# Performance work log

Hardware: AMD Instinct MI355X
Metric: run time of the kernel (lower is better)

Reference implementation:

```python
import jax, jax.numpy as jnp
import numpy as np

B, H, I = 64, 4096, 14336   # batch, hidden, expert intermediate
NLUT = 4096                 # 2**L_bits, L=12
W_SCALE = 0.02              # payload['W_scale'] (same for all three here)


def _rademacher(key, shape):
    return jnp.where(jax.random.bernoulli(key, 0.5, shape), 1.0, -1.0).astype(jnp.float32)


def setup_inputs() -> dict:
    key = jax.random.key(0)
    ks = jax.random.split(key, 14)
    inp = {
        "x": jax.random.normal(ks[0], (B, H), jnp.float32),
        "lut_gate": jax.random.normal(ks[1], (NLUT,), jnp.float32) * 0.05,
        "lut_up": jax.random.normal(ks[2], (NLUT,), jnp.float32) * 0.05,
        "lut_down": jax.random.normal(ks[3], (NLUT,), jnp.float32) * 0.05,
        "gate_walks": jax.random.randint(ks[4], (I, H), 0, NLUT, jnp.int32),
        "up_walks": jax.random.randint(ks[5], (I, H), 0, NLUT, jnp.int32),
        "down_walks": jax.random.randint(ks[6], (H, I), 0, NLUT, jnp.int32),
        "gate_sign_l": _rademacher(ks[7], (I,)),
        "gate_sign_r": _rademacher(ks[8], (H,)),
        "up_sign_l": _rademacher(ks[9], (I,)),
        "up_sign_r": _rademacher(ks[10], (H,)),
        "down_sign_l": _rademacher(ks[11], (H,)),
        "down_sign_r": _rademacher(ks[12], (I,)),
    }
    return inp


def _dequant(lut, walks, sign_l, sign_r):
    # trellis-walk LUT gather per weight element, then row/col signs and scalar scale
    # walks: (out, in) int codes; lut: (NLUT,)
    return (lut[walks] * sign_l[:, None] * sign_r[None, :]) * W_SCALE


def reference(x, lut_gate, lut_up, lut_down,
              gate_walks, up_walks, down_walks,
              gate_sign_l, gate_sign_r, up_sign_l, up_sign_r,
              down_sign_l, down_sign_r):
    W_gate = _dequant(lut_gate, gate_walks, gate_sign_l, gate_sign_r)  # (I, H)
    W_up = _dequant(lut_up, up_walks, up_sign_l, up_sign_r)            # (I, H)
    W_down = _dequant(lut_down, down_walks, down_sign_l, down_sign_r)  # (H, I)
    gate_out = jax.nn.silu(x @ W_gate.T)   # (B, I)
    up_out = x @ W_up.T                    # (B, I)
    hidden = gate_out * up_out
    return hidden @ W_down.T               # (B, H)
```

## Files before the change

kernel.cpp:

```cpp
#include <hip/hip_runtime.h>
#include <hip/hip_bf16.h>

#define HD   4096
#define ID   14336
#define NB   64
#define NLUTN 4096
#define GU_KS 4
#define D_KS  16

typedef __attribute__((ext_vector_type(8))) short short8;
typedef __attribute__((ext_vector_type(4))) float f32x4;

__device__ __forceinline__ unsigned short f2bf(float f) {
  __hip_bfloat16 h = __float2bfloat16(f);
  return __builtin_bit_cast(unsigned short, h);
}

__device__ __forceinline__ void g2l16(const unsigned short* g, unsigned short* l) {
  __builtin_amdgcn_global_load_lds(
      (const __attribute__((address_space(1))) unsigned int*)g,
      (__attribute__((address_space(3))) unsigned int*)l, 16, 0, 0);
}

__global__ __launch_bounds__(256) void prep_kernel(
    const float* __restrict__ x, const float* __restrict__ gsr,
    const float* __restrict__ usr,
    unsigned short* __restrict__ xg, unsigned short* __restrict__ xu)
{
  int t = blockIdx.x * 256 + threadIdx.x;
  float4 xv = ((const float4*)x)[t];
  int hs = t & (HD/4 - 1);
  float4 g = ((const float4*)gsr)[hs];
  float4 u = ((const float4*)usr)[hs];
  ((ushort4*)xg)[t] = make_ushort4(f2bf(xv.x*g.x), f2bf(xv.y*g.y), f2bf(xv.z*g.z), f2bf(xv.w*g.w));
  ((ushort4*)xu)[t] = make_ushort4(f2bf(xv.x*u.x), f2bf(xv.y*u.y), f2bf(xv.z*u.z), f2bf(xv.w*u.w));
}

__global__ __launch_bounds__(256, 4) void gate_up_kernel(
    const int* __restrict__ gw, const int* __restrict__ uw,
    const float* __restrict__ lutg_f, const float* __restrict__ lutu_f,
    const unsigned short* __restrict__ xg, const unsigned short* __restrict__ xu,
    float* __restrict__ pg, float* __restrict__ pu)
{
  __shared__ unsigned short lutg[NLUTN];
  __shared__ unsigned short lutu[NLUTN];
  __shared__ unsigned short Bg[2][64*32];
  __shared__ unsigned short Bu[2][64*32];

  const int tid = threadIdx.x;
  #pragma unroll
  for (int i = tid; i < NLUTN/4; i += 256) {
    float4 g = ((const float4*)lutg_f)[i];
    float4 u = ((const float4*)lutu_f)[i];
    ((ushort4*)lutg)[i] = make_ushort4(f2bf(g.x), f2bf(g.y), f2bf(g.z), f2bf(g.w));
    ((ushort4*)lutu)[i] = make_ushort4(f2bf(u.x), f2bf(u.y), f2bf(u.z), f2bf(u.w));
  }

  const int lane = tid & 63;
  const int wv   = tid >> 6;
  const int col  = lane & 15;
  const int quad = lane >> 4;
  const int m0   = blockIdx.x * 64;
  const int mrow0 = m0 + wv * 16;
  const int kb   = blockIdx.y * (HD / GU_KS);
  const int KC   = HD / GU_KS;

  const int srow = 16*wv + (lane >> 2);
  const int soff = (lane & 3) * 8;
  const unsigned short* xgs = xg + (size_t)srow * HD + kb + soff;
  const unsigned short* xus = xu + (size_t)srow * HD + kb + soff;

  const int* gp = gw + (size_t)(mrow0 + col) * HD + kb + quad * 8;
  const int* up = uw + (size_t)(mrow0 + col) * HD + kb + quad * 8;

  g2l16(xgs, &Bg[0][wv*512]);
  g2l16(xus, &Bu[0][wv*512]);
  int4 ga = *(const int4*)(gp);
  int4 gb = *(const int4*)(gp + 4);
  int4 ua = *(const int4*)(up);
  int4 ub = *(const int4*)(up + 4);
  __syncthreads();

  const f32x4 z = {0.f, 0.f, 0.f, 0.f};
  f32x4 accg[4] = {z, z, z, z};
  f32x4 accu[4] = {z, z, z, z};

  for (int k0 = 0; k0 < KC; k0 += 32) {
    const int buf = (k0 >> 5) & 1;
    const int kn = k0 + 32;
    if (kn < KC) {
      g2l16(xgs + kn, &Bg[buf^1][wv*512]);
      g2l16(xus + kn, &Bu[buf^1][wv*512]);
    }
    int4 cga = ga, cgb = gb, cua = ua, cub = ub;
    const int knw = (kn < KC) ? kn : 0;
    ga = *(const int4*)(gp + knw);
    gb = *(const int4*)(gp + knw + 4);
    ua = *(const int4*)(up + knw);
    ub = *(const int4*)(up + knw + 4);

    short8 afg, afu;
    afg[0] = (short)lutg[cga.x]; afg[1] = (short)lutg[cga.y];
    afg[2] = (short)lutg[cga.z]; afg[3] = (short)lutg[cga.w];
    afg[4] = (short)lutg[cgb.x]; afg[5] = (short)lutg[cgb.y];
    afg[6] = (short)lutg[cgb.z]; afg[7] = (short)lutg[cgb.w];
    afu[0] = (short)lutu[cua.x]; afu[1] = (short)lutu[cua.y];
    afu[2] = (short)lutu[cua.z]; afu[3] = (short)lutu[cua.w];
    afu[4] = (short)lutu[cub.x]; afu[5] = (short)lutu[cub.y];
    afu[6] = (short)lutu[cub.z]; afu[7] = (short)lutu[cub.w];

    #pragma unroll
    for (int t = 0; t < 4; ++t) {
      short8 bgf = *(const short8*)&Bg[buf][(t*16 + col)*32 + quad*8];
      short8 buf_ = *(const short8*)&Bu[buf][(t*16 + col)*32 + quad*8];
      accg[t] = __builtin_amdgcn_mfma_f32_16x16x32_bf16(afg, bgf, accg[t], 0, 0, 0);
      accu[t] = __builtin_amdgcn_mfma_f32_16x16x32_bf16(afu, buf_, accu[t], 0, 0, 0);
    }
    __syncthreads();
  }

  const int irow = mrow0 + quad * 4;
  #pragma unroll
  for (int t = 0; t < 4; ++t) {
    const int b = t*16 + col;
    float* pgb = pg + (size_t)b * ID + irow;
    float* pub = pu + (size_t)b * ID + irow;
    #pragma unroll
    for (int r = 0; r < 4; ++r) {
      atomicAdd(pgb + r, accg[t][r]);
      atomicAdd(pub + r, accu[t][r]);
    }
  }
}

__global__ __launch_bounds__(256) void hidden_kernel(
    const float* __restrict__ pg, const float* __restrict__ pu,
    const float* __restrict__ gsl, const float* __restrict__ usl,
    const float* __restrict__ dsr,
    unsigned short* __restrict__ hidden)
{
  const int t = blockIdx.x * 256 + threadIdx.x;
  const int I4 = ID / 4;
  const int b = t / I4, i4 = t % I4;
  float4 g4 = ((const float4*)pg)[(size_t)b * I4 + i4];
  float4 u4 = ((const float4*)pu)[(size_t)b * I4 + i4];
  float4 sg = ((const float4*)gsl)[i4];
  float4 su = ((const float4*)usl)[i4];
  float4 sd = ((const float4*)dsr)[i4];
  float g0 = g4.x * 0.02f * sg.x, u0 = u4.x * 0.02f * su.x;
  float g1 = g4.y * 0.02f * sg.y, u1 = u4.y * 0.02f * su.y;
  float g2 = g4.z * 0.02f * sg.z, u2 = u4.z * 0.02f * su.z;
  float g3 = g4.w * 0.02f * sg.w, u3 = u4.w * 0.02f * su.w;
  ushort4 hv;
  hv.x = f2bf((g0 / (1.f + __expf(-g0))) * u0 * sd.x);
  hv.y = f2bf((g1 / (1.f + __expf(-g1))) * u1 * sd.y);
  hv.z = f2bf((g2 / (1.f + __expf(-g2))) * u2 * sd.z);
  hv.w = f2bf((g3 / (1.f + __expf(-g3))) * u3 * sd.w);
  ((ushort4*)hidden)[(size_t)b * I4 + i4] = hv;
}

__global__ __launch_bounds__(256, 4) void down_kernel(
    const int* __restrict__ dw, const float* __restrict__ lutd_f,
    const unsigned short* __restrict__ hidden,
    const float* __restrict__ dsl,
    float* __restrict__ out)
{
  __shared__ unsigned short lutd[NLUTN];
  __shared__ unsigned short Bh[2][64*32];

  const int tid = threadIdx.x;
  #pragma unroll
  for (int i = tid; i < NLUTN/4; i += 256) {
    float4 d = ((const float4*)lutd_f)[i];
    ((ushort4*)lutd)[i] = make_ushort4(f2bf(d.x), f2bf(d.y), f2bf(d.z), f2bf(d.w));
  }

  const int lane = tid & 63;
  const int wv   = tid >> 6;
  const int col  = lane & 15;
  const int quad = lane >> 4;
  const int m0   = blockIdx.x * 64;
  const int mrow0 = m0 + wv * 16;
  const int kb   = blockIdx.y * (ID / D_KS);
  const int KC   = ID / D_KS;

  const int srow = 16*wv + (lane >> 2);
  const int soff = (lane & 3) * 8;
  const unsigned short* hsrc = hidden + (size_t)srow * ID + kb + soff;

  const int* dp = dw + (size_t)(mrow0 + col) * ID + kb + quad * 8;

  g2l16(hsrc, &Bh[0][wv*512]);
  int4 da = *(const int4*)(dp);
  int4 db = *(const int4*)(dp + 4);
  __syncthreads();

  const f32x4 z = {0.f, 0.f, 0.f, 0.f};
  f32x4 acc[4] = {z, z, z, z};

  for (int k0 = 0; k0 < KC; k0 += 32) {
    const int buf = (k0 >> 5) & 1;
    const int kn = k0 + 32;
    if (kn < KC) g2l16(hsrc + kn, &Bh[buf^1][wv*512]);
    int4 cda = da, cdb = db;
    const int knw = (kn < KC) ? kn : 0;
    da = *(const int4*)(dp + knw);
    db = *(const int4*)(dp + knw + 4);

    short8 af;
    af[0] = (short)lutd[cda.x]; af[1] = (short)lutd[cda.y];
    af[2] = (short)lutd[cda.z]; af[3] = (short)lutd[cda.w];
    af[4] = (short)lutd[cdb.x]; af[5] = (short)lutd[cdb.y];
    af[6] = (short)lutd[cdb.z]; af[7] = (short)lutd[cdb.w];

    #pragma unroll
    for (int t = 0; t < 4; ++t) {
      short8 bh = *(const short8*)&Bh[buf][(t*16 + col)*32 + quad*8];
      acc[t] = __builtin_amdgcn_mfma_f32_16x16x32_bf16(af, bh, acc[t], 0, 0, 0);
    }
    __syncthreads();
  }

  const int hrow = mrow0 + quad * 4;
  float sc[4];
  #pragma unroll
  for (int r = 0; r < 4; ++r) sc[r] = 0.02f * dsl[hrow + r];
  #pragma unroll
  for (int t = 0; t < 4; ++t) {
    const int b = t*16 + col;
    float* ob = out + (size_t)b * HD + hrow;
    #pragma unroll
    for (int r = 0; r < 4; ++r)
      atomicAdd(ob + r, acc[t][r] * sc[r]);
  }
}

extern "C" void kernel_launch(void* const* d_in, const int* in_sizes, int n_in,
                              void* d_out, int out_size, void* d_ws, size_t ws_size,
                              hipStream_t stream) {
  const float* x    = (const float*)d_in[0];
  const float* lutg = (const float*)d_in[1];
  const float* lutu = (const float*)d_in[2];
  const float* lutd = (const float*)d_in[3];
  const int*   gw   = (const int*)d_in[4];
  const int*   uw   = (const int*)d_in[5];
  const int*   dw   = (const int*)d_in[6];
  const float* gsl  = (const float*)d_in[7];
  const float* gsr  = (const float*)d_in[8];
  const float* usl  = (const float*)d_in[9];
  const float* usr  = (const float*)d_in[10];
  const float* dsl  = (const float*)d_in[11];
  const float* dsr  = (const float*)d_in[12];
  float* out = (float*)d_out;

  unsigned short* xg     = (unsigned short*)d_ws;
  unsigned short* xu     = xg + (size_t)NB * HD;
  unsigned short* hidden = xu + (size_t)NB * HD;
  float* pg = (float*)(hidden + (size_t)NB * ID);
  float* pu = pg + (size_t)NB * ID;

  hipMemsetAsync(d_out, 0, (size_t)NB * HD * sizeof(float), stream);
  hipMemsetAsync(pg, 0, (size_t)2 * NB * ID * sizeof(float), stream);
  prep_kernel<<<(NB*HD/4 + 255)/256, 256, 0, stream>>>(x, gsr, usr, xg, xu);
  gate_up_kernel<<<dim3(ID/64, GU_KS), 256, 0, stream>>>(gw, uw, lutg, lutu,
                                                         xg, xu, pg, pu);
  hidden_kernel<<<(NB*ID/4 + 255)/256, 256, 0, stream>>>(pg, pu, gsl, usl, dsr,
                                                         hidden);
  down_kernel<<<dim3(HD/64, D_KS), 256, 0, stream>>>(dw, lutd, hidden, dsl, out);
}
```

Baseline: 757.6 us.

## Load activation fragments directly from global into registers, drop LDS staging and barriers

The gate/up and down kernels no longer stage activation tiles through double-buffered shared memory with global_load_lds. Each lane now reads its MFMA B-operand fragments straight from global memory into registers, prefetching the next k-step while the MFMAs run. This removes the per-iteration __syncthreads and the LDS traffic. In exchange every wave loads the full 64-row activation tile itself, so global/L2 reads go up by the number of waves per block, and register pressure rises. A barrier is added after the LUT fill so the lookups read a fully written table.

```diff
diff --git a/kernel.cpp b/kernel.cpp
--- a/kernel.cpp
+++ b/kernel.cpp
@@ -14,12 +14,6 @@
 __device__ __forceinline__ unsigned short f2bf(float f) {
   __hip_bfloat16 h = __float2bfloat16(f);
   return __builtin_bit_cast(unsigned short, h);
-}
-
-__device__ __forceinline__ void g2l16(const unsigned short* g, unsigned short* l) {
-  __builtin_amdgcn_global_load_lds(
-      (const __attribute__((address_space(1))) unsigned int*)g,
-      (__attribute__((address_space(3))) unsigned int*)l, 16, 0, 0);
 }
 
 __global__ __launch_bounds__(256) void prep_kernel(
@@ -44,8 +38,6 @@
 {
   __shared__ unsigned short lutg[NLUTN];
   __shared__ unsigned short lutu[NLUTN];
-  __shared__ unsigned short Bg[2][64*32];
-  __shared__ unsigned short Bu[2][64*32];
 
   const int tid = threadIdx.x;
   #pragma unroll
@@ -55,6 +47,7 @@
     ((ushort4*)lutg)[i] = make_ushort4(f2bf(g.x), f2bf(g.y), f2bf(g.z), f2bf(g.w));
     ((ushort4*)lutu)[i] = make_ushort4(f2bf(u.x), f2bf(u.y), f2bf(u.z), f2bf(u.w));
   }
+  __syncthreads();
 
   const int lane = tid & 63;
   const int wv   = tid >> 6;
@@ -65,58 +58,55 @@
   const int kb   = blockIdx.y * (HD / GU_KS);
   const int KC   = HD / GU_KS;
 
-  const int srow = 16*wv + (lane >> 2);
-  const int soff = (lane & 3) * 8;
-  const unsigned short* xgs = xg + (size_t)srow * HD + kb + soff;
-  const unsigned short* xus = xu + (size_t)srow * HD + kb + soff;
-
   const int* gp = gw + (size_t)(mrow0 + col) * HD + kb + quad * 8;
   const int* up = uw + (size_t)(mrow0 + col) * HD + kb + quad * 8;
-
-  g2l16(xgs, &Bg[0][wv*512]);
-  g2l16(xus, &Bu[0][wv*512]);
+  const unsigned short* xgp[4];
+  const unsigned short* xup[4];
+  #pragma unroll
+  for (int t = 0; t < 4; ++t) {
+    xgp[t] = xg + (size_t)(t*16 + col) * HD + kb + quad * 8;
+    xup[t] = xu + (size_t)(t*16 + col) * HD + kb + quad * 8;
+  }
+
   int4 ga = *(const int4*)(gp);
   int4 gb = *(const int4*)(gp + 4);
   int4 ua = *(const int4*)(up);
   int4 ub = *(const int4*)(up + 4);
-  __syncthreads();
+  short8 bgr[4], bur[4];
+  #pragma unroll
+  for (int t = 0; t < 4; ++t) {
+    bgr[t] = __builtin_bit_cast(short8, *(const int4*)(xgp[t]));
+    bur[t] = __builtin_bit_cast(short8, *(const int4*)(xup[t]));
+  }
 
   const f32x4 z = {0.f, 0.f, 0.f, 0.f};
   f32x4 accg[4] = {z, z, z, z};
   f32x4 accu[4] = {z, z, z, z};
 
   for (int k0 = 0; k0 < KC; k0 += 32) {
-    const int buf = (k0 >> 5) & 1;
-    const int kn = k0 + 32;
-    if (kn < KC) {
-      g2l16(xgs + kn, &Bg[buf^1][wv*512]);
-      g2l16(xus + kn, &Bu[buf^1][wv*512]);
+    short8 afg, afu;
+    afg[0] = (short)lutg[ga.x]; afg[1] = (short)lutg[ga.y];
+    afg[2] = (short)lutg[ga.z]; afg[3] = (short)lutg[ga.w];
+    afg[4] = (short)lutg[gb.x]; afg[5] = (short)lutg[gb.y];
+    afg[6] = (short)lutg[gb.z]; afg[7] = (short)lutg[gb.w];
+    afu[0] = (short)lutu[ua.x]; afu[1] = (short)lutu[ua.y];
+    afu[2] = (short)lutu[ua.z]; afu[3] = (short)lutu[ua.w];
+    afu[4] = (short)lutu[ub.x]; afu[5] = (short)lutu[ub.y];
+    afu[6] = (short)lutu[ub.z]; afu[7] = (short)lutu[ub.w];
+
+    const int kn = (k0 + 32 < KC) ? (k0 + 32) : 0;
+    ga = *(const int4*)(gp + kn);
+    gb = *(const int4*)(gp + kn + 4);
+    ua = *(const int4*)(up + kn);
+    ub = *(const int4*)(up + kn + 4);
+
+    #pragma unroll
+    for (int t = 0; t < 4; ++t) {
+      accg[t] = __builtin_amdgcn_mfma_f32_16x16x32_bf16(afg, bgr[t], accg[t], 0, 0, 0);
+      accu[t] = __builtin_amdgcn_mfma_f32_16x16x32_bf16(afu, bur[t], accu[t], 0, 0, 0);
+      bgr[t] = __builtin_bit_cast(short8, *(const int4*)(xgp[t] + kn));
+      bur[t] = __builtin_bit_cast(short8, *(const int4*)(xup[t] + kn));
     }
-    int4 cga = ga, cgb = gb, cua = ua, cub = ub;
-    const int knw = (kn < KC) ? kn : 0;
-    ga = *(const int4*)(gp + knw);
-    gb = *(const int4*)(gp + knw + 4);
-    ua = *(const int4*)(up + knw);
-    ub = *(const int4*)(up + knw + 4);
-
-    short8 afg, afu;
-    afg[0] = (short)lutg[cga.x]; afg[1] = (short)lutg[cga.y];
-    afg[2] = (short)lutg[cga.z]; afg[3] = (short)lutg[cga.w];
-    afg[4] = (short)lutg[cgb.x]; afg[5] = (short)lutg[cgb.y];
-    afg[6] = (short)lutg[cgb.z]; afg[7] = (short)lutg[cgb.w];
-    afu[0] = (short)lutu[cua.x]; afu[1] = (short)lutu[cua.y];
-    afu[2] = (short)lutu[cua.z]; afu[3] = (short)lutu[cua.w];
-    afu[4] = (short)lutu[cub.x]; afu[5] = (short)lutu[cub.y];
-    afu[6] = (short)lutu[cub.z]; afu[7] = (short)lutu[cub.w];
-
-    #pragma unroll
-    for (int t = 0; t < 4; ++t) {
-      short8 bgf = *(const short8*)&Bg[buf][(t*16 + col)*32 + quad*8];
-      short8 buf_ = *(const short8*)&Bu[buf][(t*16 + col)*32 + quad*8];
-      accg[t] = __builtin_amdgcn_mfma_f32_16x16x32_bf16(afg, bgf, accg[t], 0, 0, 0);
-      accu[t] = __builtin_amdgcn_mfma_f32_16x16x32_bf16(afu, buf_, accu[t], 0, 0, 0);
-    }
-    __syncthreads();
   }
 
   const int irow = mrow0 + quad * 4;
@@ -166,7 +156,6 @@
     float* __restrict__ out)
 {
   __shared__ unsigned short lutd[NLUTN];
-  __shared__ unsigned short Bh[2][64*32];
 
   const int tid = threadIdx.x;
   #pragma unroll
@@ -174,6 +163,7 @@
     float4 d = ((const float4*)lutd_f)[i];
     ((ushort4*)lutd)[i] = make_ushort4(f2bf(d.x), f2bf(d.y), f2bf(d.z), f2bf(d.w));
   }
+  __syncthreads();
 
   const int lane = tid & 63;
   const int wv   = tid >> 6;
@@ -184,41 +174,38 @@
   const int kb   = blockIdx.y * (ID / D_KS);
   const int KC   = ID / D_KS;
 
-  const int srow = 16*wv + (lane >> 2);
-  const int soff = (lane & 3) * 8;
-  const unsigned short* hsrc = hidden + (size_t)srow * ID + kb + soff;
-
   const int* dp = dw + (size_t)(mrow0 + col) * ID + kb + quad * 8;
-
-  g2l16(hsrc, &Bh[0][wv*512]);
+  const unsigned short* hp[4];
+  #pragma unroll
+  for (int t = 0; t < 4; ++t)
+    hp[t] = hidden + (size_t)(t*16 + col) * ID + kb + quad * 8;
+
   int4 da = *(const int4*)(dp);
   int4 db = *(const int4*)(dp + 4);
-  __syncthreads();
+  short8 bhr[4];
+  #pragma unroll
+  for (int t = 0; t < 4; ++t)
+    bhr[t] = __builtin_bit_cast(short8, *(const int4*)(hp[t]));
 
   const f32x4 z = {0.f, 0.f, 0.f, 0.f};
   f32x4 acc[4] = {z, z, z, z};
 
   for (int k0 = 0; k0 < KC; k0 += 32) {
-    const int buf = (k0 >> 5) & 1;
-    const int kn = k0 + 32;
-    if (kn < KC) g2l16(hsrc + kn, &Bh[buf^1][wv*512]);
-    int4 cda = da, cdb = db;
-    const int knw = (kn < KC) ? kn : 0;
-    da = *(const int4*)(dp + knw);
-    db = *(const int4*)(dp + knw + 4);
-
     short8 af;
-    af[0] = (short)lutd[cda.x]; af[1] = (short)lutd[cda.y];
-    af[2] = (short)lutd[cda.z]; af[3] = (short)lutd[cda.w];
-    af[4] = (short)lutd[cdb.x]; af[5] = (short)lutd[cdb.y];
-    af[6] = (short)lutd[cdb.z]; af[7] = (short)lutd[cdb.w];
+    af[0] = (short)lutd[da.x]; af[1] = (short)lutd[da.y];
+    af[2] = (short)lutd[da.z]; af[3] = (short)lutd[da.w];
+    af[4] = (short)lutd[db.x]; af[5] = (short)lutd[db.y];
+    af[6] = (short)lutd[db.z]; af[7] = (short)lutd[db.w];
+
+    const int kn = (k0 + 32 < KC) ? (k0 + 32) : 0;
+    da = *(const int4*)(dp + kn);
+    db = *(const int4*)(dp + kn + 4);
 
     #pragma unroll
     for (int t = 0; t < 4; ++t) {
-      short8 bh = *(const short8*)&Bh[buf][(t*16 + col)*32 + quad*8];
-      acc[t] = __builtin_amdgcn_mfma_f32_16x16x32_bf16(af, bh, acc[t], 0, 0, 0);
+      acc[t] = __builtin_amdgcn_mfma_f32_16x16x32_bf16(af, bhr[t], acc[t], 0, 0, 0);
+      bhr[t] = __builtin_bit_cast(short8, *(const int4*)(hp[t] + kn));
     }
-    __syncthreads();
   }
 
   const int hrow = mrow0 + quad * 4;
```

Result: slower. 824.2 us (+8.8%).
